# Kernel optimization log

Hardware: AMD Instinct MI355X
Metric: run time of the kernel (lower is better)

The kernel has to match this reference:

```python
import jax, jax.numpy as jnp
import numpy as np

E, C, FE, FS, K = 8, 1024, 1024, 4096, 2  # n_experts, embed, expert_inter, shared_inter, top_k
B, T = 4, 2048

def setup_inputs() -> dict:
    key = jax.random.key(0)
    ks = jax.random.split(key, 8)
    def init(k, shape, fan_in):
        return jax.random.normal(k, shape, jnp.float32) / np.sqrt(fan_in).astype(np.float32)
    return dict(
        x=jax.random.normal(ks[0], (B, T, C), jnp.float32),
        gate_w=init(ks[1], (E, C), C),        # nn.Linear(C, E, bias=False).weight
        ew1=init(ks[2], (E, C, FE), C),       # per-expert ln1 weights (transposed)
        ew2=init(ks[3], (E, C, FE), C),       # per-expert ln2 weights
        ewp=init(ks[4], (E, FE, C), FE),      # per-expert proj weights
        sw1=init(ks[5], (C, FS), C),          # shared FFN ln1
        sw2=init(ks[6], (C, FS), C),          # shared FFN ln2
        swp=init(ks[7], (FS, C), FS),         # shared FFN proj
    )

def reference(x, gate_w, ew1, ew2, ewp, sw1, sw2, swp):
    Bd, Td, Cd = x.shape
    xf = x.reshape(-1, Cd)                               # [N, C]
    scores = xf @ gate_w.T                               # [N, E] (eval mode: no noise)
    probs = jax.nn.softmax(scores, axis=-1)
    weights, indices = jax.lax.top_k(probs, K)           # [N, K]
    N = xf.shape[0]
    # combine[n, e] = routing weight of expert e for token n (0 if not selected)
    combine = jnp.zeros((N, E), xf.dtype).at[jnp.arange(N)[:, None], indices].add(weights)
    y = jnp.zeros_like(xf)
    for i in range(E):  # fixed small expert count; masked-dense replaces torch gather/scatter
        h = jax.nn.silu(xf @ ew1[i]) * (xf @ ew2[i])     # [N, FE] SwiGLU
        y = y + (h @ ewp[i]) * combine[:, i:i + 1]
    z = (jax.nn.silu(xf @ sw1) * (xf @ sw2)) @ swp       # shared expert (dropout p=0)
    return (y + z).reshape(Bd, Td, Cd), scores
```

## Files before the change

### kernel.cpp

```cpp
#include <hip/hip_runtime.h>

typedef unsigned short u16;
typedef unsigned int u32;
typedef __bf16 bf16x8 __attribute__((ext_vector_type(8)));
typedef float f32x4 __attribute__((ext_vector_type(4)));
typedef u16 u16x8 __attribute__((ext_vector_type(8)));

#define NTOK 8192
#define CDIM 1024
#define NEXP 8
#define FEDIM 1024
#define FSDIM 4096

#define GLD16(gp, lp) __builtin_amdgcn_global_load_lds( \
    (const __attribute__((address_space(1))) void*)(gp), \
    (__attribute__((address_space(3))) void*)(lp), 16, 0, 0)

__device__ __forceinline__ u16 f2bf(float f) {
  u32 u = __float_as_uint(f);
  u += 0x7FFFu + ((u >> 16) & 1u);
  return (u16)(u >> 16);
}

__device__ __forceinline__ void transpose64_body(
    const float* __restrict__ src, u16* __restrict__ dst,
    int R, int C, int bx, int by)
{
  __shared__ float tile[64][33];
  int c0 = bx * 32, r0 = by * 64;
  int tx = threadIdx.x & 31, ty = threadIdx.x >> 5;
#pragma unroll
  for (int p = 0; p < 8; p++) {
    int r = ty + p * 8;
    tile[r][tx] = src[(size_t)(r0 + r) * C + c0 + tx];
  }
  __syncthreads();
#pragma unroll
  for (int p = 0; p < 4; p++) {
    int cc = ty + p * 8;
    u32 v = (u32)f2bf(tile[2 * tx][cc]) | ((u32)f2bf(tile[2 * tx + 1][cc]) << 16);
    *(u32*)&dst[(size_t)(c0 + cc) * R + r0 + 2 * tx] = v;
  }
}

__global__ __launch_bounds__(256) void prep_kernel(
    const float* __restrict__ x, const float* __restrict__ gw,
    const float* __restrict__ ew1, const float* __restrict__ ew2,
    const float* __restrict__ ewp, const float* __restrict__ sw1,
    const float* __restrict__ sw2, const float* __restrict__ swp,
    float* __restrict__ scores, u16* __restrict__ xb, int* __restrict__ cnt,
    int* __restrict__ tok, float* __restrict__ wgt,
    u16* __restrict__ eall, u16* __restrict__ s12t, u16* __restrict__ swpt)
{
  int bid = blockIdx.x;
  if (bid >= 256) {
    int tb = bid - 256;
    if (tb < 12288) {
      int z = tb >> 9, r = tb & 511;
      const float* src = (z < 8) ? ew1 : ((z < 16) ? ew2 : ewp);
      transpose64_body(src + (size_t)(z & 7) * CDIM * FEDIM,
                       eall + (size_t)z * CDIM * FEDIM,
                       CDIM, FEDIM, r & 31, r >> 5);
    } else if (tb < 16384) {
      int i2 = tb - 12288;
      int z = i2 >> 11, r = i2 & 2047;
      transpose64_body(z ? sw2 : sw1, s12t + (size_t)z * CDIM * FSDIM,
                       CDIM, FSDIM, r & 127, r >> 7);
    } else {
      int r = tb - 16384;
      transpose64_body(swp, swpt, FSDIM, CDIM, r & 31, r >> 5);
    }
    return;
  }

  int gb = bid;
  __shared__ float smat[32][9];
  __shared__ int lcnt[NEXP];
  __shared__ int lbase[NEXP];
  __shared__ int rec_i[32];
  __shared__ int rec_p1[32], rec_p2[32];
  __shared__ float rec_w1[32], rec_w2[32];

  int tid = threadIdx.x, wave = tid >> 6, lane = tid & 63;
  if (tid < NEXP) lcnt[tid] = 0;
  __syncthreads();

  int tbase = gb * 32 + wave * 8;
#pragma unroll
  for (int it = 0; it < 8; ++it) {
    int n = tbase + it;
    const float4* xr = (const float4*)(x + (size_t)n * CDIM) + lane * 4;
    float4 xv[4];
#pragma unroll
    for (int j = 0; j < 4; j++) xv[j] = xr[j];
    u16x8 rA, rB;
    rA[0]=f2bf(xv[0].x); rA[1]=f2bf(xv[0].y); rA[2]=f2bf(xv[0].z); rA[3]=f2bf(xv[0].w);
    rA[4]=f2bf(xv[1].x); rA[5]=f2bf(xv[1].y); rA[6]=f2bf(xv[1].z); rA[7]=f2bf(xv[1].w);
    rB[0]=f2bf(xv[2].x); rB[1]=f2bf(xv[2].y); rB[2]=f2bf(xv[2].z); rB[3]=f2bf(xv[2].w);
    rB[4]=f2bf(xv[3].x); rB[5]=f2bf(xv[3].y); rB[6]=f2bf(xv[3].z); rB[7]=f2bf(xv[3].w);
    u16* xrow = xb + (size_t)n * CDIM + lane * 16;
    *(u16x8*)xrow = rA;
    *(u16x8*)(xrow + 8) = rB;

    float s[NEXP];
#pragma unroll
    for (int e = 0; e < NEXP; e++) {
      const float4* g = (const float4*)(gw + (size_t)e * CDIM) + lane * 4;
      float a = 0.f;
#pragma unroll
      for (int j = 0; j < 4; j++) {
        float4 gv = g[j];
        a += xv[j].x * gv.x + xv[j].y * gv.y + xv[j].z * gv.z + xv[j].w * gv.w;
      }
#pragma unroll
      for (int o = 32; o > 0; o >>= 1) a += __shfl_xor(a, o);
      s[e] = a;
    }
    if (lane == 0) {
      int slot = wave * 8 + it;
#pragma unroll
      for (int e = 0; e < NEXP; e++) {
        scores[(size_t)n * NEXP + e] = s[e];
        smat[slot][e] = s[e];
      }
    }
  }
  __syncthreads();

  if (tid < 32) {
    float p[NEXP];
    float m = smat[tid][0];
#pragma unroll
    for (int e = 1; e < NEXP; e++) m = fmaxf(m, smat[tid][e]);
    float sum = 0.f;
#pragma unroll
    for (int e = 0; e < NEXP; e++) { p[e] = __expf(smat[tid][e] - m); sum += p[e]; }
    int i1 = 0;
#pragma unroll
    for (int e = 1; e < NEXP; e++) if (p[e] > p[i1]) i1 = e;
    int i2 = (i1 == 0) ? 1 : 0;
#pragma unroll
    for (int e = 0; e < NEXP; e++) if (e != i1 && p[e] > p[i2]) i2 = e;
    rec_i[tid] = i1 | (i2 << 8);
    rec_w1[tid] = p[i1] / sum;
    rec_w2[tid] = p[i2] / sum;
    rec_p1[tid] = atomicAdd(&lcnt[i1], 1);
    rec_p2[tid] = atomicAdd(&lcnt[i2], 1);
  }
  __syncthreads();
  if (tid < NEXP) lbase[tid] = atomicAdd(&cnt[tid], lcnt[tid]);
  __syncthreads();
  if (tid < 32) {
    int n = gb * 32 + tid;
    int i1 = rec_i[tid] & 0xff, i2 = rec_i[tid] >> 8;
    int q1 = lbase[i1] + rec_p1[tid];
    int q2 = lbase[i2] + rec_p2[tid];
    tok[i1 * NTOK + q1] = n; wgt[i1 * NTOK + q1] = rec_w1[tid];
    tok[i2 * NTOK + q2] = n; wgt[i2 * NTOK + q2] = rec_w2[tid];
  }
}

#define BM 128
#define BN 128
#define BK 32
#define TILE (BM * BK)

template<int AMODE>
__global__ __launch_bounds__(256, 2) void gemm_swiglu(
    const u16* __restrict__ A, int lda,
    const u16* __restrict__ B1, const u16* __restrict__ B2,
    size_t bstride, int ldb,
    int M, int K,
    u16* __restrict__ H, int ldh,
    const int* __restrict__ cnt, const int* __restrict__ tok)
{
  int e = blockIdx.z;
  int Mloc = (AMODE == 0) ? M : cnt[e];
  int mbase = blockIdx.y * BM;
  if (AMODE != 0 && mbase >= Mloc) return;
  int nbase = blockIdx.x * BN;
  int tid = threadIdx.x, wid = tid >> 6, lane = tid & 63;

  __shared__ __align__(16) u16 As[2][TILE];
  __shared__ __align__(16) u16 Bs1[2][TILE];
  __shared__ __align__(16) u16 Bs2[2][TILE];

  int sr = lane >> 2;
  int kg = (lane & 3) * 8;
  int arow0 = wid * 32 + sr;
  int arow1 = arow0 + 16;

  int pfx = 0;
  if (AMODE != 0) for (int i = 0; i < NEXP; i++) pfx += (i < e) ? cnt[i] : 0;

  size_t r0, r1;
  if (AMODE == 0) {
    r0 = mbase + arow0; r1 = mbase + arow1;
  } else {
    r0 = tok[e * NTOK + min(mbase + arow0, Mloc - 1)];
    r1 = tok[e * NTOK + min(mbase + arow1, Mloc - 1)];
  }
  const u16* Ap0 = A + r0 * (size_t)lda + kg;
  const u16* Ap1 = A + r1 * (size_t)lda + kg;
  size_t boff = (AMODE != 0) ? (size_t)e * bstride : 0;
  const u16* B1p0 = B1 + boff + (size_t)(nbase + arow0) * ldb + kg;
  const u16* B1p1 = B1 + boff + (size_t)(nbase + arow1) * ldb + kg;
  const u16* B2p0 = B2 + boff + (size_t)(nbase + arow0) * ldb + kg;
  const u16* B2p1 = B2 + boff + (size_t)(nbase + arow1) * ldb + kg;

  int ldsw0 = (wid * 32) * BK;
  int ldsw1 = (wid * 32 + 16) * BK;

  int wr = wid >> 1, wc = wid & 1;
  int fr = lane & 15, fgk = (lane >> 4) * 8;

  f32x4 acc1[4][4] = {};
  f32x4 acc2[4][4] = {};

  int nt = K / BK;
  GLD16(Ap0,  &As [0][ldsw0]); GLD16(Ap1,  &As [0][ldsw1]);
  GLD16(B1p0, &Bs1[0][ldsw0]); GLD16(B1p1, &Bs1[0][ldsw1]);
  GLD16(B2p0, &Bs2[0][ldsw0]); GLD16(B2p1, &Bs2[0][ldsw1]);
  Ap0 += BK; Ap1 += BK; B1p0 += BK; B1p1 += BK; B2p0 += BK; B2p1 += BK;
  __syncthreads();

  int cur = 0;
  for (int t = 0; t < nt; ++t) {
    int nxt = cur ^ 1;
    if (t + 1 < nt) {
      GLD16(Ap0,  &As [nxt][ldsw0]); GLD16(Ap1,  &As [nxt][ldsw1]);
      GLD16(B1p0, &Bs1[nxt][ldsw0]); GLD16(B1p1, &Bs1[nxt][ldsw1]);
      GLD16(B2p0, &Bs2[nxt][ldsw0]); GLD16(B2p1, &Bs2[nxt][ldsw1]);
      Ap0 += BK; Ap1 += BK; B1p0 += BK; B1p1 += BK; B2p0 += BK; B2p1 += BK;
    }
    const u16* as = As[cur];
    const u16* b1s = Bs1[cur];
    const u16* b2s = Bs2[cur];
    bf16x8 af[4], b1f[4], b2f[4];
#pragma unroll
    for (int m = 0; m < 4; m++)
      af[m] = *(const bf16x8*)&as[(wr * 64 + m * 16 + fr) * BK + fgk];
#pragma unroll
    for (int n = 0; n < 4; n++) {
      b1f[n] = *(const bf16x8*)&b1s[(wc * 64 + n * 16 + fr) * BK + fgk];
      b2f[n] = *(const bf16x8*)&b2s[(wc * 64 + n * 16 + fr) * BK + fgk];
    }
#pragma unroll
    for (int m = 0; m < 4; m++)
#pragma unroll
      for (int n = 0; n < 4; n++) {
        acc1[m][n] = __builtin_amdgcn_mfma_f32_16x16x32_bf16(af[m], b1f[n], acc1[m][n], 0, 0, 0);
        acc2[m][n] = __builtin_amdgcn_mfma_f32_16x16x32_bf16(af[m], b2f[n], acc2[m][n], 0, 0, 0);
      }
    __syncthreads();
    cur = nxt;
  }

  int fg4 = (lane >> 4) * 4;
#pragma unroll
  for (int m = 0; m < 4; m++) {
#pragma unroll
    for (int j = 0; j < 4; j++) {
      int rloc = wr * 64 + m * 16 + fg4 + j;
      int rr = mbase + rloc;
      if (AMODE != 0 && rr >= Mloc) continue;
      size_t orow = (size_t)(pfx + rr);
#pragma unroll
      for (int n = 0; n < 4; n++) {
        int col = nbase + wc * 64 + n * 16 + fr;
        float g = acc1[m][n][j];
        float v = acc2[m][n][j];
        float hv = (g / (1.f + __expf(-g))) * v;
        H[orow * (size_t)ldh + col] = f2bf(hv);
      }
    }
  }
}

template<int EPI, int AMODE>
__global__ __launch_bounds__(256, 3) void gemm_proj(
    const u16* __restrict__ A, int lda,
    const u16* __restrict__ B, size_t bstride, int ldb,
    int M, int K,
    float* __restrict__ outF, int ldo,
    const int* __restrict__ cnt, const int* __restrict__ tok,
    const float* __restrict__ wgt)
{
  int e = blockIdx.z;
  int Mloc = (AMODE == 0) ? M : cnt[e];
  int mbase = blockIdx.y * BM;
  if (AMODE != 0 && mbase >= Mloc) return;
  int nbase = blockIdx.x * BN;
  int tid = threadIdx.x, wid = tid >> 6, lane = tid & 63;

  __shared__ __align__(16) u16 As[2][TILE];
  __shared__ __align__(16) u16 Bs[2][TILE];

  int sr = lane >> 2;
  int kg = (lane & 3) * 8;
  int arow0 = wid * 32 + sr;
  int arow1 = arow0 + 16;

  int pfx = 0;
  if (AMODE != 0) for (int i = 0; i < NEXP; i++) pfx += (i < e) ? cnt[i] : 0;

  size_t r0, r1;
  if (AMODE == 0) {
    r0 = mbase + arow0; r1 = mbase + arow1;
  } else {
    r0 = pfx + min(mbase + arow0, Mloc - 1);
    r1 = pfx + min(mbase + arow1, Mloc - 1);
  }
  const u16* Ap0 = A + r0 * (size_t)lda + kg;
  const u16* Ap1 = A + r1 * (size_t)lda + kg;
  const u16* Bb = B + ((AMODE != 0) ? (size_t)e * bstride : 0);
  const u16* Bp0 = Bb + (size_t)(nbase + arow0) * ldb + kg;
  const u16* Bp1 = Bb + (size_t)(nbase + arow1) * ldb + kg;

  int ldsw0 = (wid * 32) * BK;
  int ldsw1 = (wid * 32 + 16) * BK;

  int wr = wid >> 1, wc = wid & 1;
  int fr = lane & 15, fgk = (lane >> 4) * 8;

  f32x4 acc[4][4] = {};

  int nt = K / BK;
  GLD16(Ap0, &As[0][ldsw0]); GLD16(Ap1, &As[0][ldsw1]);
  GLD16(Bp0, &Bs[0][ldsw0]); GLD16(Bp1, &Bs[0][ldsw1]);
  Ap0 += BK; Ap1 += BK; Bp0 += BK; Bp1 += BK;
  __syncthreads();

  int cur = 0;
  for (int t = 0; t < nt; ++t) {
    int nxt = cur ^ 1;
    if (t + 1 < nt) {
      GLD16(Ap0, &As[nxt][ldsw0]); GLD16(Ap1, &As[nxt][ldsw1]);
      GLD16(Bp0, &Bs[nxt][ldsw0]); GLD16(Bp1, &Bs[nxt][ldsw1]);
      Ap0 += BK; Ap1 += BK; Bp0 += BK; Bp1 += BK;
    }
    const u16* as = As[cur];
    const u16* bs = Bs[cur];
    bf16x8 af[4], bfr[4];
#pragma unroll
    for (int m = 0; m < 4; m++)
      af[m] = *(const bf16x8*)&as[(wr * 64 + m * 16 + fr) * BK + fgk];
#pragma unroll
    for (int n = 0; n < 4; n++)
      bfr[n] = *(const bf16x8*)&bs[(wc * 64 + n * 16 + fr) * BK + fgk];
#pragma unroll
    for (int m = 0; m < 4; m++)
#pragma unroll
      for (int n = 0; n < 4; n++)
        acc[m][n] = __builtin_amdgcn_mfma_f32_16x16x32_bf16(af[m], bfr[n], acc[m][n], 0, 0, 0);
    __syncthreads();
    cur = nxt;
  }

  int fg4 = (lane >> 4) * 4;
#pragma unroll
  for (int m = 0; m < 4; m++) {
#pragma unroll
    for (int j = 0; j < 4; j++) {
      int rloc = wr * 64 + m * 16 + fg4 + j;
      int rr = mbase + rloc;
      if (AMODE != 0 && rr >= Mloc) continue;
      int t = 0; float wv = 0.f;
      if (EPI == 4) { t = tok[e * NTOK + rr]; wv = wgt[e * NTOK + rr]; }
#pragma unroll
      for (int n = 0; n < 4; n++) {
        int col = nbase + wc * 64 + n * 16 + fr;
        float v = acc[m][n][j];
        if (EPI == 2) {
          outF[(size_t)rr * ldo + col] = v;
        } else {
          unsafeAtomicAdd(&outF[(size_t)t * ldo + col], v * wv);
        }
      }
    }
  }
}

extern "C" void kernel_launch(void* const* d_in, const int* in_sizes, int n_in,
                              void* d_out, int out_size, void* d_ws, size_t ws_size,
                              hipStream_t stream)
{
  const float* x   = (const float*)d_in[0];
  const float* gw  = (const float*)d_in[1];
  const float* ew1 = (const float*)d_in[2];
  const float* ew2 = (const float*)d_in[3];
  const float* ewp = (const float*)d_in[4];
  const float* sw1 = (const float*)d_in[5];
  const float* sw2 = (const float*)d_in[6];
  const float* swp = (const float*)d_in[7];
  float* out    = (float*)d_out;
  float* scores = out + (size_t)NTOK * CDIM;

  char* wsp = (char*)d_ws;
  size_t off = 0;
  auto alloc = [&](size_t bytes) -> void* {
    void* p = wsp + off; off += (bytes + 255) & ~(size_t)255; return p;
  };
  u16* xb   = (u16*)alloc((size_t)NTOK * CDIM * 2);
  u16* eall = (u16*)alloc((size_t)24 * CDIM * FEDIM * 2);
  u16* ew1t = eall;
  u16* ew2t = eall + (size_t)8 * CDIM * FEDIM;
  u16* ewpt = eall + (size_t)16 * CDIM * FEDIM;
  u16* s12t = (u16*)alloc((size_t)2 * FSDIM * CDIM * 2);
  u16* sw1t = s12t;
  u16* sw2t = s12t + (size_t)FSDIM * CDIM;
  u16* swpt = (u16*)alloc((size_t)CDIM * FSDIM * 2);
  u16* hs   = (u16*)alloc((size_t)NTOK * FSDIM * 2);
  u16* he   = hs;
  int* cnt  = (int*)alloc(256);
  int* tok  = (int*)alloc((size_t)NEXP * NTOK * 4);
  float* wgt = (float*)alloc((size_t)NEXP * NTOK * 4);
  if (off > ws_size) return;

  hipMemsetAsync(cnt, 0, 32, stream);

  prep_kernel<<<18688, 256, 0, stream>>>(x, gw, ew1, ew2, ewp, sw1, sw2, swp,
                                         scores, xb, cnt, tok, wgt,
                                         eall, s12t, swpt);

  gemm_swiglu<0><<<dim3(FSDIM/BN, NTOK/BM, 1), 256, 0, stream>>>(
      xb, CDIM, sw1t, sw2t, 0, CDIM, NTOK, CDIM, hs, FSDIM, nullptr, nullptr);
  gemm_proj<2,0><<<dim3(CDIM/BN, NTOK/BM, 1), 256, 0, stream>>>(
      hs, FSDIM, swpt, 0, FSDIM, NTOK, FSDIM, out, CDIM, nullptr, nullptr, nullptr);

  size_t estride = (size_t)FEDIM * CDIM;
  gemm_swiglu<1><<<dim3(FEDIM/BN, NTOK/BM, NEXP), 256, 0, stream>>>(
      xb, CDIM, ew1t, ew2t, estride, CDIM, 0, CDIM, he, FEDIM, cnt, tok);
  gemm_proj<4,2><<<dim3(CDIM/BN, NTOK/BM, NEXP), 256, 0, stream>>>(
      he, FEDIM, ewpt, estride, FEDIM, 0, FEDIM, out, CDIM, cnt, tok, wgt);
}
```

Before: 556.9 us.

## Interleave gate and up weights into a single GEMM with SwiGLU via lane shuffle

The transpose step now writes the w1 and w2 weight rows interleaved, so each output column pair holds a gate and an up value. A single unified GEMM kernel computes both at once over a doubled N dimension, and its epilogue pairs adjacent lanes with a shuffle to apply SiLU times up and store half the columns. This drops the dual-accumulator kernel, halving accumulator registers and LDS per block so occupancy can rise to 3 blocks per CU. The trade-off is that the A tile is reused over half as many output columns per block, and half the lanes sit idle during the store.

Result: slower. 593.8 us (+6.6%).

```diff
diff --git a/kernel.cpp b/kernel.cpp
--- a/kernel.cpp
+++ b/kernel.cpp
@@ -40,6 +40,30 @@
     int cc = ty + p * 8;
     u32 v = (u32)f2bf(tile[2 * tx][cc]) | ((u32)f2bf(tile[2 * tx + 1][cc]) << 16);
     *(u32*)&dst[(size_t)(c0 + cc) * R + r0 + 2 * tx] = v;
+  }
+}
+
+__device__ __forceinline__ void transpose_i64_body(
+    const float* __restrict__ s1, const float* __restrict__ s2,
+    u16* __restrict__ dst, int R, int C, int bx, int by)
+{
+  __shared__ float t1[64][33], t2[64][33];
+  int c0 = bx * 32, r0 = by * 64;
+  int tx = threadIdx.x & 31, ty = threadIdx.x >> 5;
+#pragma unroll
+  for (int p = 0; p < 8; p++) {
+    int r = ty + p * 8;
+    t1[r][tx] = s1[(size_t)(r0 + r) * C + c0 + tx];
+    t2[r][tx] = s2[(size_t)(r0 + r) * C + c0 + tx];
+  }
+  __syncthreads();
+#pragma unroll
+  for (int p = 0; p < 4; p++) {
+    int cc = ty + p * 8;
+    u32 v1 = (u32)f2bf(t1[2 * tx][cc]) | ((u32)f2bf(t1[2 * tx + 1][cc]) << 16);
+    u32 v2 = (u32)f2bf(t2[2 * tx][cc]) | ((u32)f2bf(t2[2 * tx + 1][cc]) << 16);
+    *(u32*)&dst[(size_t)(2 * (c0 + cc) + 0) * R + r0 + 2 * tx] = v1;
+    *(u32*)&dst[(size_t)(2 * (c0 + cc) + 1) * R + r0 + 2 * tx] = v2;
   }
 }
 
@@ -50,25 +74,30 @@
     const float* __restrict__ sw2, const float* __restrict__ swp,
     float* __restrict__ scores, u16* __restrict__ xb, int* __restrict__ cnt,
     int* __restrict__ tok, float* __restrict__ wgt,
-    u16* __restrict__ eall, u16* __restrict__ s12t, u16* __restrict__ swpt)
+    u16* __restrict__ ewi, u16* __restrict__ swi,
+    u16* __restrict__ swpt, u16* __restrict__ ewpt)
 {
   int bid = blockIdx.x;
   if (bid >= 256) {
     int tb = bid - 256;
-    if (tb < 12288) {
-      int z = tb >> 9, r = tb & 511;
-      const float* src = (z < 8) ? ew1 : ((z < 16) ? ew2 : ewp);
-      transpose64_body(src + (size_t)(z & 7) * CDIM * FEDIM,
-                       eall + (size_t)z * CDIM * FEDIM,
-                       CDIM, FEDIM, r & 31, r >> 5);
-    } else if (tb < 16384) {
-      int i2 = tb - 12288;
-      int z = i2 >> 11, r = i2 & 2047;
-      transpose64_body(z ? sw2 : sw1, s12t + (size_t)z * CDIM * FSDIM,
-                       CDIM, FSDIM, r & 127, r >> 7);
+    if (tb < 4096) {
+      int e = tb >> 9, r = tb & 511;
+      transpose_i64_body(ew1 + (size_t)e * CDIM * FEDIM,
+                         ew2 + (size_t)e * CDIM * FEDIM,
+                         ewi + (size_t)e * 2 * FEDIM * CDIM,
+                         CDIM, FEDIM, r & 31, r >> 5);
+    } else if (tb < 6144) {
+      int r = tb - 4096;
+      transpose_i64_body(sw1, sw2, swi, CDIM, FSDIM, r & 127, r >> 7);
+    } else if (tb < 8192) {
+      int r = tb - 6144;
+      transpose64_body(swp, swpt, FSDIM, CDIM, r & 31, r >> 5);
     } else {
-      int r = tb - 16384;
-      transpose64_body(swp, swpt, FSDIM, CDIM, r & 31, r >> 5);
+      int t4 = tb - 8192;
+      int z = t4 >> 9, r = t4 & 511;
+      transpose64_body(ewp + (size_t)z * FEDIM * CDIM,
+                       ewpt + (size_t)z * CDIM * FEDIM,
+                       FEDIM, CDIM, r & 31, r >> 5);
     }
     return;
   }
@@ -165,14 +194,15 @@
 #define BK 32
 #define TILE (BM * BK)
 
-template<int AMODE>
-__global__ __launch_bounds__(256, 2) void gemm_swiglu(
+template<int EPI, int AMODE>
+__global__ __launch_bounds__(256, 3) void gemm_u(
     const u16* __restrict__ A, int lda,
-    const u16* __restrict__ B1, const u16* __restrict__ B2,
-    size_t bstride, int ldb,
+    const u16* __restrict__ B, size_t bstride, int ldb,
     int M, int K,
-    u16* __restrict__ H, int ldh,
-    const int* __restrict__ cnt, const int* __restrict__ tok)
+    u16* __restrict__ Hout, int ldh,
+    float* __restrict__ outF, int ldo,
+    const int* __restrict__ cnt, const int* __restrict__ tok,
+    const float* __restrict__ wgt)
 {
   int e = blockIdx.z;
   int Mloc = (AMODE == 0) ? M : cnt[e];
@@ -182,8 +212,7 @@
   int tid = threadIdx.x, wid = tid >> 6, lane = tid & 63;
 
   __shared__ __align__(16) u16 As[2][TILE];
-  __shared__ __align__(16) u16 Bs1[2][TILE];
-  __shared__ __align__(16) u16 Bs2[2][TILE];
+  __shared__ __align__(16) u16 Bs[2][TILE];
 
   int sr = lane >> 2;
   int kg = (lane & 3) * 8;
@@ -196,117 +225,9 @@
   size_t r0, r1;
   if (AMODE == 0) {
     r0 = mbase + arow0; r1 = mbase + arow1;
-  } else {
+  } else if (AMODE == 1) {
     r0 = tok[e * NTOK + min(mbase + arow0, Mloc - 1)];
     r1 = tok[e * NTOK + min(mbase + arow1, Mloc - 1)];
-  }
-  const u16* Ap0 = A + r0 * (size_t)lda + kg;
-  const u16* Ap1 = A + r1 * (size_t)lda + kg;
-  size_t boff = (AMODE != 0) ? (size_t)e * bstride : 0;
-  const u16* B1p0 = B1 + boff + (size_t)(nbase + arow0) * ldb + kg;
-  const u16* B1p1 = B1 + boff + (size_t)(nbase + arow1) * ldb + kg;
-  const u16* B2p0 = B2 + boff + (size_t)(nbase + arow0) * ldb + kg;
-  const u16* B2p1 = B2 + boff + (size_t)(nbase + arow1) * ldb + kg;
-
-  int ldsw0 = (wid * 32) * BK;
-  int ldsw1 = (wid * 32 + 16) * BK;
-
-  int wr = wid >> 1, wc = wid & 1;
-  int fr = lane & 15, fgk = (lane >> 4) * 8;
-
-  f32x4 acc1[4][4] = {};
-  f32x4 acc2[4][4] = {};
-
-  int nt = K / BK;
-  GLD16(Ap0,  &As [0][ldsw0]); GLD16(Ap1,  &As [0][ldsw1]);
-  GLD16(B1p0, &Bs1[0][ldsw0]); GLD16(B1p1, &Bs1[0][ldsw1]);
-  GLD16(B2p0, &Bs2[0][ldsw0]); GLD16(B2p1, &Bs2[0][ldsw1]);
-  Ap0 += BK; Ap1 += BK; B1p0 += BK; B1p1 += BK; B2p0 += BK; B2p1 += BK;
-  __syncthreads();
-
-  int cur = 0;
-  for (int t = 0; t < nt; ++t) {
-    int nxt = cur ^ 1;
-    if (t + 1 < nt) {
-      GLD16(Ap0,  &As [nxt][ldsw0]); GLD16(Ap1,  &As [nxt][ldsw1]);
-      GLD16(B1p0, &Bs1[nxt][ldsw0]); GLD16(B1p1, &Bs1[nxt][ldsw1]);
-      GLD16(B2p0, &Bs2[nxt][ldsw0]); GLD16(B2p1, &Bs2[nxt][ldsw1]);
-      Ap0 += BK; Ap1 += BK; B1p0 += BK; B1p1 += BK; B2p0 += BK; B2p1 += BK;
-    }
-    const u16* as = As[cur];
-    const u16* b1s = Bs1[cur];
-    const u16* b2s = Bs2[cur];
-    bf16x8 af[4], b1f[4], b2f[4];
-#pragma unroll
-    for (int m = 0; m < 4; m++)
-      af[m] = *(const bf16x8*)&as[(wr * 64 + m * 16 + fr) * BK + fgk];
-#pragma unroll
-    for (int n = 0; n < 4; n++) {
-      b1f[n] = *(const bf16x8*)&b1s[(wc * 64 + n * 16 + fr) * BK + fgk];
-      b2f[n] = *(const bf16x8*)&b2s[(wc * 64 + n * 16 + fr) * BK + fgk];
-    }
-#pragma unroll
-    for (int m = 0; m < 4; m++)
-#pragma unroll
-      for (int n = 0; n < 4; n++) {
-        acc1[m][n] = __builtin_amdgcn_mfma_f32_16x16x32_bf16(af[m], b1f[n], acc1[m][n], 0, 0, 0);
-        acc2[m][n] = __builtin_amdgcn_mfma_f32_16x16x32_bf16(af[m], b2f[n], acc2[m][n], 0, 0, 0);
-      }
-    __syncthreads();
-    cur = nxt;
-  }
-
-  int fg4 = (lane >> 4) * 4;
-#pragma unroll
-  for (int m = 0; m < 4; m++) {
-#pragma unroll
-    for (int j = 0; j < 4; j++) {
-      int rloc = wr * 64 + m * 16 + fg4 + j;
-      int rr = mbase + rloc;
-      if (AMODE != 0 && rr >= Mloc) continue;
-      size_t orow = (size_t)(pfx + rr);
-#pragma unroll
-      for (int n = 0; n < 4; n++) {
-        int col = nbase + wc * 64 + n * 16 + fr;
-        float g = acc1[m][n][j];
-        float v = acc2[m][n][j];
-        float hv = (g / (1.f + __expf(-g))) * v;
-        H[orow * (size_t)ldh + col] = f2bf(hv);
-      }
-    }
-  }
-}
-
-template<int EPI, int AMODE>
-__global__ __launch_bounds__(256, 3) void gemm_proj(
-    const u16* __restrict__ A, int lda,
-    const u16* __restrict__ B, size_t bstride, int ldb,
-    int M, int K,
-    float* __restrict__ outF, int ldo,
-    const int* __restrict__ cnt, const int* __restrict__ tok,
-    const float* __restrict__ wgt)
-{
-  int e = blockIdx.z;
-  int Mloc = (AMODE == 0) ? M : cnt[e];
-  int mbase = blockIdx.y * BM;
-  if (AMODE != 0 && mbase >= Mloc) return;
-  int nbase = blockIdx.x * BN;
-  int tid = threadIdx.x, wid = tid >> 6, lane = tid & 63;
-
-  __shared__ __align__(16) u16 As[2][TILE];
-  __shared__ __align__(16) u16 Bs[2][TILE];
-
-  int sr = lane >> 2;
-  int kg = (lane & 3) * 8;
-  int arow0 = wid * 32 + sr;
-  int arow1 = arow0 + 16;
-
-  int pfx = 0;
-  if (AMODE != 0) for (int i = 0; i < NEXP; i++) pfx += (i < e) ? cnt[i] : 0;
-
-  size_t r0, r1;
-  if (AMODE == 0) {
-    r0 = mbase + arow0; r1 = mbase + arow1;
   } else {
     r0 = pfx + min(mbase + arow0, Mloc - 1);
     r1 = pfx + min(mbase + arow1, Mloc - 1);
@@ -365,16 +286,23 @@
       int rloc = wr * 64 + m * 16 + fg4 + j;
       int rr = mbase + rloc;
       if (AMODE != 0 && rr >= Mloc) continue;
-      int t = 0; float wv = 0.f;
-      if (EPI == 4) { t = tok[e * NTOK + rr]; wv = wgt[e * NTOK + rr]; }
+      int tk = 0; float wv = 0.f;
+      if (EPI == 4) { tk = tok[e * NTOK + rr]; wv = wgt[e * NTOK + rr]; }
 #pragma unroll
       for (int n = 0; n < 4; n++) {
         int col = nbase + wc * 64 + n * 16 + fr;
         float v = acc[m][n][j];
-        if (EPI == 2) {
+        if (EPI == 0) {
+          float o = __shfl_xor(v, 1);
+          float g  = (fr & 1) ? o : v;
+          float vv = (fr & 1) ? v : o;
+          float hv = (g / (1.f + __expf(-g))) * vv;
+          if (!(fr & 1))
+            Hout[(size_t)(pfx + rr) * ldh + (col >> 1)] = f2bf(hv);
+        } else if (EPI == 2) {
           outF[(size_t)rr * ldo + col] = v;
         } else {
-          unsafeAtomicAdd(&outF[(size_t)t * ldo + col], v * wv);
+          unsafeAtomicAdd(&outF[(size_t)tk * ldo + col], v * wv);
         }
       }
     }
@@ -402,14 +330,10 @@
     void* p = wsp + off; off += (bytes + 255) & ~(size_t)255; return p;
   };
   u16* xb   = (u16*)alloc((size_t)NTOK * CDIM * 2);
-  u16* eall = (u16*)alloc((size_t)24 * CDIM * FEDIM * 2);
-  u16* ew1t = eall;
-  u16* ew2t = eall + (size_t)8 * CDIM * FEDIM;
-  u16* ewpt = eall + (size_t)16 * CDIM * FEDIM;
-  u16* s12t = (u16*)alloc((size_t)2 * FSDIM * CDIM * 2);
-  u16* sw1t = s12t;
-  u16* sw2t = s12t + (size_t)FSDIM * CDIM;
+  u16* ewi  = (u16*)alloc((size_t)NEXP * 2 * FEDIM * CDIM * 2);
+  u16* swi  = (u16*)alloc((size_t)2 * FSDIM * CDIM * 2);
   u16* swpt = (u16*)alloc((size_t)CDIM * FSDIM * 2);
+  u16* ewpt = (u16*)alloc((size_t)NEXP * CDIM * FEDIM * 2);
   u16* hs   = (u16*)alloc((size_t)NTOK * FSDIM * 2);
   u16* he   = hs;
   int* cnt  = (int*)alloc(256);
@@ -419,18 +343,21 @@
 
   hipMemsetAsync(cnt, 0, 32, stream);
 
-  prep_kernel<<<18688, 256, 0, stream>>>(x, gw, ew1, ew2, ewp, sw1, sw2, swp,
+  prep_kernel<<<12544, 256, 0, stream>>>(x, gw, ew1, ew2, ewp, sw1, sw2, swp,
                                          scores, xb, cnt, tok, wgt,
-                                         eall, s12t, swpt);
-
-  gemm_swiglu<0><<<dim3(FSDIM/BN, NTOK/BM, 1), 256, 0, stream>>>(
-      xb, CDIM, sw1t, sw2t, 0, CDIM, NTOK, CDIM, hs, FSDIM, nullptr, nullptr);
-  gemm_proj<2,0><<<dim3(CDIM/BN, NTOK/BM, 1), 256, 0, stream>>>(
-      hs, FSDIM, swpt, 0, FSDIM, NTOK, FSDIM, out, CDIM, nullptr, nullptr, nullptr);
-
-  size_t estride = (size_t)FEDIM * CDIM;
-  gemm_swiglu<1><<<dim3(FEDIM/BN, NTOK/BM, NEXP), 256, 0, stream>>>(
-      xb, CDIM, ew1t, ew2t, estride, CDIM, 0, CDIM, he, FEDIM, cnt, tok);
-  gemm_proj<4,2><<<dim3(CDIM/BN, NTOK/BM, NEXP), 256, 0, stream>>>(
-      he, FEDIM, ewpt, estride, FEDIM, 0, FEDIM, out, CDIM, cnt, tok, wgt);
-}
+                                         ewi, swi, swpt, ewpt);
+
+  gemm_u<0,0><<<dim3(2*FSDIM/BN, NTOK/BM, 1), 256, 0, stream>>>(
+      xb, CDIM, swi, 0, CDIM, NTOK, CDIM, hs, FSDIM, nullptr, 0,
+      nullptr, nullptr, nullptr);
+  gemm_u<2,0><<<dim3(CDIM/BN, NTOK/BM, 1), 256, 0, stream>>>(
+      hs, FSDIM, swpt, 0, FSDIM, NTOK, FSDIM, nullptr, 0, out, CDIM,
+      nullptr, nullptr, nullptr);
+
+  gemm_u<0,1><<<dim3(2*FEDIM/BN, NTOK/BM, NEXP), 256, 0, stream>>>(
+      xb, CDIM, ewi, (size_t)2 * FEDIM * CDIM, CDIM, 0, CDIM, he, FEDIM,
+      nullptr, 0, cnt, tok, nullptr);
+  gemm_u<4,2><<<dim3(CDIM/BN, NTOK/BM, NEXP), 256, 0, stream>>>(
+      he, FEDIM, ewpt, (size_t)CDIM * FEDIM, FEDIM, 0, FEDIM, nullptr, 0,
+      out, CDIM, cnt, tok, wgt);
+}
```
